# Kernel tuning notes

Measured on AMD Instinct MI355X. Metric: run time of the kernel, lower is better.

Reference implementation:

```python
import jax, jax.numpy as jnp
import numpy as np

N_NODES = 100000


def setup_inputs() -> dict:
    key = jax.random.key(0)
    k1, k2, k3, k4 = jax.random.split(key, 4)
    E = 1600000
    in_dim, out_dim = 256, 64
    h = jax.random.normal(k1, (N_NODES, in_dim), dtype=jnp.float32)
    src = jax.random.randint(k2, (E,), 0, N_NODES, dtype=jnp.int64)
    dst = jax.random.randint(k3, (E,), 0, N_NODES, dtype=jnp.int64)
    W = jax.random.normal(k4, (in_dim, out_dim), dtype=jnp.float32) * (1.0 / np.sqrt(in_dim))
    b = jnp.zeros((out_dim,), dtype=jnp.float32)
    return {"h": h, "src": src, "dst": dst, "W": W, "b": b}


def reference(h, src, dst, W, b):
    # dgl GraphConv, norm='both': out = D_in^{-1/2} A D_out^{-1/2} h W + b
    E = src.shape[0]
    ones = jnp.ones((E,), dtype=h.dtype)
    deg_out = jax.ops.segment_sum(ones, src, num_segments=N_NODES)  # out-degree of src nodes
    deg_in = jax.ops.segment_sum(ones, dst, num_segments=N_NODES)   # in-degree of dst nodes
    norm_src = jnp.clip(deg_out, 1.0, None) ** -0.5                  # [N]
    norm_dst = jnp.clip(deg_in, 1.0, None) ** -0.5                   # [N]
    # in_dim > out_dim: project first (as dgl does), then aggregate small features
    x = (h * norm_src[:, None]) @ W                                  # [N, out_dim]
    msgs = x[src]                                                    # [E, out_dim] gather
    agg = jax.ops.segment_sum(msgs, dst, num_segments=N_NODES)      # [N, out_dim] scatter-add
    out = agg * norm_dst[:, None] + b
    # ReLU; dropout is identity in eval mode
    return jax.nn.relu(out)
```

## Files before the change

### kernel.cpp

```cpp
#include <hip/hip_runtime.h>
#include <hip/hip_fp16.h>

#define N_NODES 100000
#define IN_DIM 256
#define OUT_DIM 64
#define NT 782
#define NSC 512
#define SMAX 3200
#define CAP_F 3072
#define GEMM_BLKS 1563
#define NSPLIT 4
#define A_LD 136
#define FUSED_LDS 47568

typedef _Float16 half8 __attribute__((ext_vector_type(8)));
typedef float f32x4 __attribute__((ext_vector_type(4)));

__global__ __launch_bounds__(256) void init_kernel(int* __restrict__ cursorD,
                                                   int* __restrict__ cursorS) {
    int i = blockIdx.x * 256 + threadIdx.x;
    if (i < NT) { cursorD[i] = 0; cursorS[i] = 0; }
}

__global__ __launch_bounds__(256) void fused_kernel(const int* __restrict__ src,
                                                    const int* __restrict__ dst,
                                                    int* __restrict__ cursorD,
                                                    int* __restrict__ cursorS,
                                                    int* __restrict__ binnedD,
                                                    unsigned char* __restrict__ srcb,
                                                    const float* __restrict__ hmat,
                                                    const float* __restrict__ W,
                                                    __half* __restrict__ xh,
                                                    int E, int chunk) {
    __shared__ char smem[FUSED_LDS];
    const int t = threadIdx.x;
    if (blockIdx.x < NSC) {
        int* sorted            = (int*)(smem);
        int* histD             = (int*)(smem + 12800);
        int* boffD             = (int*)(smem + 15928);
        int* resvD             = (int*)(smem + 19056);
        int* histS             = (int*)(smem + 22184);
        int* boffS             = (int*)(smem + 25312);
        int* resvS             = (int*)(smem + 28440);
        unsigned short* sbin   = (unsigned short*)(smem + 31568);
        unsigned short* sbinS  = (unsigned short*)(smem + 37968);
        unsigned char* sortedB = (unsigned char*)(smem + 44368);
        const int blk = blockIdx.x;
        const int lane = t & 63, wv = t >> 6;
        const int lo = blk * chunk;
        int hiA = lo + chunk; if (hiA > E) hiA = E;
        for (int s0 = lo; s0 < hiA; s0 += SMAX) {
            int m = hiA - s0; if (m > SMAX) m = SMAX;
            for (int i = t; i < NT; i += 256) { histD[i] = 0; histS[i] = 0; }
            __syncthreads();
            for (int k = t; k < m; k += 256) {
                int s = src[s0 + k], d = dst[s0 + k];
                atomicAdd(&histD[d >> 7], 1);
                atomicAdd(&histS[s >> 7], 1);
            }
            __syncthreads();
            if (wv < 2) {
                int* hsrc = (wv == 0) ? histD : histS;
                int* bdst = (wv == 0) ? boffD : boffS;
                int carry = 0;
                for (int r = 0; r < (NT + 63) / 64; ++r) {
                    int i = r * 64 + lane;
                    int v = (i < NT) ? hsrc[i] : 0;
                    int incl = v;
#pragma unroll
                    for (int off = 1; off < 64; off <<= 1) {
                        int y = __shfl_up(incl, off);
                        if (lane >= off) incl += y;
                    }
                    if (i < NT) bdst[i] = carry + incl - v;
                    carry += __shfl(incl, 63);
                }
            }
            __syncthreads();
            for (int i = t; i < NT; i += 256) {
                int hd = histD[i];
                if (hd) resvD[i] = atomicAdd(&cursorD[i], hd);
                int hs = histS[i];
                if (hs) resvS[i] = atomicAdd(&cursorS[i], hs);
                histD[i] = boffD[i];
                histS[i] = boffS[i];
            }
            __syncthreads();
            for (int k = t; k < m; k += 256) {
                int s = src[s0 + k], d = dst[s0 + k];
                int bd = d >> 7;
                int p = atomicAdd(&histD[bd], 1);
                sorted[p] = (s << 7) | (d & 127);
                sbin[p] = (unsigned short)bd;
                int bs = s >> 7;
                int ps = atomicAdd(&histS[bs], 1);
                sortedB[ps] = (unsigned char)(s & 127);
                sbinS[ps] = (unsigned short)bs;
            }
            __syncthreads();
            for (int k = t; k < m; k += 256) {
                int b = sbin[k];
                int loc = resvD[b] + (k - boffD[b]);
                if (loc < CAP_F) binnedD[b * CAP_F + loc] = sorted[k];
                int bs = sbinS[k];
                int locS = resvS[bs] + (k - boffS[bs]);
                if (locS < CAP_F) srcb[bs * CAP_F + locS] = sortedB[k];
            }
            __syncthreads();
        }
    } else {
        _Float16* sA = (_Float16*)(smem);
        _Float16* sB = (_Float16*)(smem + 64 * A_LD * 2);
        const int lane = t & 63;
        const int w = t >> 6;
        const int row0 = (blockIdx.x - NSC) * 64;
        const int m0 = (w & 1) * 32;
        const int n0 = (w >> 1) * 32;

        f32x4 acc00 = {0.f, 0.f, 0.f, 0.f}, acc01 = {0.f, 0.f, 0.f, 0.f};
        f32x4 acc10 = {0.f, 0.f, 0.f, 0.f}, acc11 = {0.f, 0.f, 0.f, 0.f};

        for (int khalf = 0; khalf < 2; ++khalf) {
            const int k0 = khalf * 128;
            __syncthreads();
#pragma unroll
            for (int it = 0; it < 8; ++it) {
                int f = t + it * 256;
                int row = f >> 5;
                int c4 = f & 31;
                int grow = row0 + row; if (grow >= N_NODES) grow = N_NODES - 1;
                float4 v = *(const float4*)(hmat + (size_t)grow * IN_DIM + k0 + c4 * 4);
                _Float16 p[4];
                p[0] = (_Float16)v.x; p[1] = (_Float16)v.y;
                p[2] = (_Float16)v.z; p[3] = (_Float16)v.w;
                *(uint2*)&sA[row * A_LD + c4 * 4] = *(uint2*)p;
            }
            {
                int n = t & 63;
                int kk0 = (t >> 6) * 32;
#pragma unroll
                for (int kb = 0; kb < 8; ++kb) {
                    _Float16 p[4];
#pragma unroll
                    for (int u = 0; u < 4; ++u)
                        p[u] = (_Float16)W[(size_t)(k0 + kk0 + kb * 4 + u) * OUT_DIM + n];
                    *(uint2*)&sB[n * A_LD + kk0 + kb * 4] = *(uint2*)p;
                }
            }
            __syncthreads();
#pragma unroll
            for (int kb = 0; kb < 4; ++kb) {
                int koff = kb * 32 + (lane >> 4) * 8;
                half8 a0 = *(const half8*)&sA[(m0 + (lane & 15)) * A_LD + koff];
                half8 a1 = *(const half8*)&sA[(m0 + 16 + (lane & 15)) * A_LD + koff];
                half8 b0 = *(const half8*)&sB[(n0 + (lane & 15)) * A_LD + koff];
                half8 b1 = *(const half8*)&sB[(n0 + 16 + (lane & 15)) * A_LD + koff];
                acc00 = __builtin_amdgcn_mfma_f32_16x16x32_f16(a0, b0, acc00, 0, 0, 0);
                acc01 = __builtin_amdgcn_mfma_f32_16x16x32_f16(a0, b1, acc01, 0, 0, 0);
                acc10 = __builtin_amdgcn_mfma_f32_16x16x32_f16(a1, b0, acc10, 0, 0, 0);
                acc11 = __builtin_amdgcn_mfma_f32_16x16x32_f16(a1, b1, acc11, 0, 0, 0);
            }
        }

        const int col16 = lane & 15;
        const int rq = (lane >> 4) * 4;
#pragma unroll
        for (int mi = 0; mi < 2; ++mi) {
#pragma unroll
            for (int ni = 0; ni < 2; ++ni) {
                const f32x4 a = (mi == 0) ? (ni == 0 ? acc00 : acc01)
                                          : (ni == 0 ? acc10 : acc11);
                int col = n0 + ni * 16 + col16;
#pragma unroll
                for (int r = 0; r < 4; ++r) {
                    int row = row0 + m0 + mi * 16 + rq + r;
                    if (row < N_NODES)
                        xh[(size_t)row * OUT_DIM + col] = __float2half(a[r]);
                }
            }
        }
    }
}

__global__ __launch_bounds__(256) void scale_kernel(const int* __restrict__ cursorS,
                                                    const unsigned char* __restrict__ srcb,
                                                    __half* __restrict__ xh) {
    __shared__ int h[128];
    __shared__ float sc[128];
    const int bin = blockIdx.x, t = threadIdx.x;
    if (t < 128) h[t] = 0;
    __syncthreads();
    int ms = cursorS[bin]; if (ms > CAP_F) ms = CAP_F;
    const int sbase = bin * CAP_F;
    for (int k = t; k < ms; k += 256) atomicAdd(&h[srcb[sbase + k]], 1);
    __syncthreads();
    if (t < 128) {
        int d = h[t];
        sc[t] = rsqrtf((float)(d < 1 ? 1 : d));
    }
    __syncthreads();
    const int node0 = bin * 128;
    for (int i = t; i < 128 * 16; i += 256) {
        int r = i >> 4, q = i & 15;
        int node = node0 + r;
        if (node < N_NODES) {
            __half2* p = (__half2*)(xh + (size_t)node * OUT_DIM + q * 4);
            float s = sc[r];
            __half2 a0 = p[0], a1 = p[1];
            float2 f0 = __half22float2(a0), f1 = __half22float2(a1);
            __half2 r0, r1;
            r0.x = __float2half(f0.x * s); r0.y = __float2half(f0.y * s);
            r1.x = __float2half(f1.x * s); r1.y = __float2half(f1.y * s);
            p[0] = r0; p[1] = r1;
        }
    }
}

__global__ __launch_bounds__(256) void agg_kernel(const int* __restrict__ cursorD,
                                                  const int* __restrict__ binnedD,
                                                  const __half* __restrict__ xh,
                                                  const float* __restrict__ b,
                                                  float* __restrict__ out) {
    __shared__ int lcsr[CAP_F];
    __shared__ int h[128], cur[128], loff[128], lcnt[128];
    __shared__ int w0tot;
    const int bin = blockIdx.x / NSPLIT;
    const int part = blockIdx.x % NSPLIT;
    const int t = threadIdx.x, lane = t & 63, wv = t >> 6;

    if (t < 128) h[t] = 0;
    __syncthreads();
    const int base = bin * CAP_F;
    int m = cursorD[bin]; if (m > CAP_F) m = CAP_F;
    for (int k = t; k < m; k += 256) atomicAdd(&h[binnedD[base + k] & 127], 1);
    __syncthreads();
    int v = (t < 128) ? h[t] : 0;
    int incl = v;
#pragma unroll
    for (int off = 1; off < 64; off <<= 1) {
        int y = __shfl_up(incl, off);
        if (lane >= off) incl += y;
    }
    if (t == 63) w0tot = incl;
    __syncthreads();
    int excl = incl - v + ((t >= 64 && t < 128) ? w0tot : 0);
    if (t < 128) { loff[t] = excl; lcnt[t] = v; cur[t] = excl; }
    __syncthreads();
    for (int k = t; k < m; k += 256) {
        int rec = binnedD[base + k];
        int p = atomicAdd(&cur[rec & 127], 1);
        lcsr[p] = rec >> 7;
    }
    __syncthreads();

    const int g = lane >> 3;
    const int c = lane & 7;
    for (int idx = 0; idx < 8; ++idx) {
        const int nloc = part * 32 + wv * 8 + idx;
        const int node = bin * 128 + nloc;
        if (node >= N_NODES) continue;
        const int start = loff[nloc];
        const int n = lcnt[nloc];

        float acc[8] = {0.f, 0.f, 0.f, 0.f, 0.f, 0.f, 0.f, 0.f};
        for (int e0 = 0; e0 < n; e0 += 16) {
            int ea = e0 + g;
            int eb = ea + 8;
            bool va = ea < n;
            bool vb = eb < n;
            int sa0 = va ? lcsr[start + ea] : 0;
            float wa = va ? 1.f : 0.f;
            uint4 ra = *(const uint4*)(xh + (size_t)sa0 * OUT_DIM + 8 * c);
            const bool grpb = (e0 + 8) < n;
            uint4 rb;
            float wb = 0.f;
            if (grpb) {
                int sb0 = vb ? lcsr[start + eb] : 0;
                wb = vb ? 1.f : 0.f;
                rb = *(const uint4*)(xh + (size_t)sb0 * OUT_DIM + 8 * c);
            }
            {
                const __half2* hp = (const __half2*)&ra;
#pragma unroll
                for (int p = 0; p < 4; ++p) {
                    float2 f = __half22float2(hp[p]);
                    acc[2 * p]     = fmaf(wa, f.x, acc[2 * p]);
                    acc[2 * p + 1] = fmaf(wa, f.y, acc[2 * p + 1]);
                }
            }
            if (grpb) {
                const __half2* hp = (const __half2*)&rb;
#pragma unroll
                for (int p = 0; p < 4; ++p) {
                    float2 f = __half22float2(hp[p]);
                    acc[2 * p]     = fmaf(wb, f.x, acc[2 * p]);
                    acc[2 * p + 1] = fmaf(wb, f.y, acc[2 * p + 1]);
                }
            }
        }

#pragma unroll
        for (int off = 8; off < 64; off <<= 1) {
#pragma unroll
            for (int p = 0; p < 8; ++p)
                acc[p] += __shfl_xor(acc[p], off);
        }

        if (g == 0) {
            float nrm = rsqrtf((float)(n < 1 ? 1 : n));
            float4 bv0 = *(const float4*)&b[c * 8];
            float4 bv1 = *(const float4*)&b[c * 8 + 4];
            float4 r0, r1;
            r0.x = fmaxf(fmaf(acc[0], nrm, bv0.x), 0.f);
            r0.y = fmaxf(fmaf(acc[1], nrm, bv0.y), 0.f);
            r0.z = fmaxf(fmaf(acc[2], nrm, bv0.z), 0.f);
            r0.w = fmaxf(fmaf(acc[3], nrm, bv0.w), 0.f);
            r1.x = fmaxf(fmaf(acc[4], nrm, bv1.x), 0.f);
            r1.y = fmaxf(fmaf(acc[5], nrm, bv1.y), 0.f);
            r1.z = fmaxf(fmaf(acc[6], nrm, bv1.z), 0.f);
            r1.w = fmaxf(fmaf(acc[7], nrm, bv1.w), 0.f);
            float4* orow = (float4*)(out + (size_t)node * OUT_DIM + c * 8);
            orow[0] = r0;
            orow[1] = r1;
        }
    }
}

extern "C" void kernel_launch(void* const* d_in, const int* in_sizes, int n_in,
                              void* d_out, int out_size, void* d_ws, size_t ws_size,
                              hipStream_t stream) {
    const float* h   = (const float*)d_in[0];
    const int*   src = (const int*)d_in[1];
    const int*   dst = (const int*)d_in[2];
    const float* W   = (const float*)d_in[3];
    const float* b   = (const float*)d_in[4];
    float* out = (float*)d_out;
    const int E = in_sizes[1];
    const int chunkS = (E + NSC - 1) / NSC;

    char* ws = (char*)d_ws;
    int*           cursorD = (int*)(ws);
    int*           cursorS = (int*)(ws + 3328);
    int*           binnedD = (int*)(ws + 6656);
    unsigned char* srcb    = (unsigned char*)(ws + 9615872);
    __half*        xh      = (__half*)(ws + 12018176);

    init_kernel<<<4, 256, 0, stream>>>(cursorD, cursorS);
    fused_kernel<<<NSC + GEMM_BLKS, 256, 0, stream>>>(src, dst, cursorD, cursorS,
                                                      binnedD, srcb, h, W, xh, E, chunkS);
    scale_kernel<<<NT, 256, 0, stream>>>(cursorS, srcb, xh);
    agg_kernel<<<NT * NSPLIT, 256, 0, stream>>>(cursorD, binnedD, xh, b, out);
}
```

Before: 252.5 us.

## Build per-node CSR once in scale kernel, use one wave per node in aggregation

```diff
diff --git a/kernel.cpp b/kernel.cpp
--- a/kernel.cpp
+++ b/kernel.cpp
@@ -9,7 +9,6 @@
 #define SMAX 3200
 #define CAP_F 3072
 #define GEMM_BLKS 1563
-#define NSPLIT 4
 #define A_LD 136
 #define FUSED_LDS 47568
 
@@ -182,12 +181,51 @@
     }
 }
 
-__global__ __launch_bounds__(256) void scale_kernel(const int* __restrict__ cursorS,
-                                                    const unsigned char* __restrict__ srcb,
-                                                    __half* __restrict__ xh) {
-    __shared__ int h[128];
+__global__ __launch_bounds__(256) void tile_scale_kernel(const int* __restrict__ cursorD,
+                                                         const int* __restrict__ cursorS,
+                                                         const int* __restrict__ binnedD,
+                                                         const unsigned char* __restrict__ srcb,
+                                                         int* __restrict__ csr,
+                                                         int* __restrict__ offs,
+                                                         int* __restrict__ cnt,
+                                                         __half* __restrict__ xh) {
+    __shared__ int h[128], cur[128];
+    __shared__ int lcsr[CAP_F];
     __shared__ float sc[128];
-    const int bin = blockIdx.x, t = threadIdx.x;
+    __shared__ int w0tot;
+    const int bin = blockIdx.x, t = threadIdx.x, lane = t & 63;
+    if (t < 128) h[t] = 0;
+    __syncthreads();
+
+    const int base = bin * CAP_F;
+    int m = cursorD[bin]; if (m > CAP_F) m = CAP_F;
+    for (int k = t; k < m; k += 256) atomicAdd(&h[binnedD[base + k] & 127], 1);
+    __syncthreads();
+    int v = (t < 128) ? h[t] : 0;
+    int incl = v;
+#pragma unroll
+    for (int off = 1; off < 64; off <<= 1) {
+        int y = __shfl_up(incl, off);
+        if (lane >= off) incl += y;
+    }
+    if (t == 63) w0tot = incl;
+    __syncthreads();
+    int excl = incl - v + ((t >= 64 && t < 128) ? w0tot : 0);
+    if (t < 128) {
+        cur[t] = excl;
+        int node = bin * 128 + t;
+        if (node < N_NODES) { offs[node] = base + excl; cnt[node] = v; }
+    }
+    __syncthreads();
+    for (int k = t; k < m; k += 256) {
+        int rec = binnedD[base + k];
+        int p = atomicAdd(&cur[rec & 127], 1);
+        lcsr[p] = rec >> 7;
+    }
+    __syncthreads();
+    for (int k = t; k < m; k += 256) csr[base + k] = lcsr[k];
+
+    __syncthreads();
     if (t < 128) h[t] = 0;
     __syncthreads();
     int ms = cursorS[bin]; if (ms > CAP_F) ms = CAP_F;
@@ -216,113 +254,82 @@
     }
 }
 
-__global__ __launch_bounds__(256) void agg_kernel(const int* __restrict__ cursorD,
-                                                  const int* __restrict__ binnedD,
+__global__ __launch_bounds__(256) void agg_kernel(const int* __restrict__ offs,
+                                                  const int* __restrict__ cnt,
+                                                  const int* __restrict__ csr,
                                                   const __half* __restrict__ xh,
                                                   const float* __restrict__ b,
                                                   float* __restrict__ out) {
-    __shared__ int lcsr[CAP_F];
-    __shared__ int h[128], cur[128], loff[128], lcnt[128];
-    __shared__ int w0tot;
-    const int bin = blockIdx.x / NSPLIT;
-    const int part = blockIdx.x % NSPLIT;
-    const int t = threadIdx.x, lane = t & 63, wv = t >> 6;
-
-    if (t < 128) h[t] = 0;
-    __syncthreads();
-    const int base = bin * CAP_F;
-    int m = cursorD[bin]; if (m > CAP_F) m = CAP_F;
-    for (int k = t; k < m; k += 256) atomicAdd(&h[binnedD[base + k] & 127], 1);
-    __syncthreads();
-    int v = (t < 128) ? h[t] : 0;
-    int incl = v;
-#pragma unroll
-    for (int off = 1; off < 64; off <<= 1) {
-        int y = __shfl_up(incl, off);
-        if (lane >= off) incl += y;
-    }
-    if (t == 63) w0tot = incl;
-    __syncthreads();
-    int excl = incl - v + ((t >= 64 && t < 128) ? w0tot : 0);
-    if (t < 128) { loff[t] = excl; lcnt[t] = v; cur[t] = excl; }
-    __syncthreads();
-    for (int k = t; k < m; k += 256) {
-        int rec = binnedD[base + k];
-        int p = atomicAdd(&cur[rec & 127], 1);
-        lcsr[p] = rec >> 7;
-    }
-    __syncthreads();
-
+    const int t = threadIdx.x;
+    const int lane = t & 63;
+    const int wid = t >> 6;
+    const int node = blockIdx.x * 4 + wid;
     const int g = lane >> 3;
     const int c = lane & 7;
-    for (int idx = 0; idx < 8; ++idx) {
-        const int nloc = part * 32 + wv * 8 + idx;
-        const int node = bin * 128 + nloc;
-        if (node >= N_NODES) continue;
-        const int start = loff[nloc];
-        const int n = lcnt[nloc];
-
-        float acc[8] = {0.f, 0.f, 0.f, 0.f, 0.f, 0.f, 0.f, 0.f};
-        for (int e0 = 0; e0 < n; e0 += 16) {
-            int ea = e0 + g;
-            int eb = ea + 8;
-            bool va = ea < n;
-            bool vb = eb < n;
-            int sa0 = va ? lcsr[start + ea] : 0;
-            float wa = va ? 1.f : 0.f;
-            uint4 ra = *(const uint4*)(xh + (size_t)sa0 * OUT_DIM + 8 * c);
-            const bool grpb = (e0 + 8) < n;
-            uint4 rb;
-            float wb = 0.f;
-            if (grpb) {
-                int sb0 = vb ? lcsr[start + eb] : 0;
-                wb = vb ? 1.f : 0.f;
-                rb = *(const uint4*)(xh + (size_t)sb0 * OUT_DIM + 8 * c);
-            }
-            {
-                const __half2* hp = (const __half2*)&ra;
-#pragma unroll
-                for (int p = 0; p < 4; ++p) {
-                    float2 f = __half22float2(hp[p]);
-                    acc[2 * p]     = fmaf(wa, f.x, acc[2 * p]);
-                    acc[2 * p + 1] = fmaf(wa, f.y, acc[2 * p + 1]);
-                }
-            }
-            if (grpb) {
-                const __half2* hp = (const __half2*)&rb;
-#pragma unroll
-                for (int p = 0; p < 4; ++p) {
-                    float2 f = __half22float2(hp[p]);
-                    acc[2 * p]     = fmaf(wb, f.x, acc[2 * p]);
-                    acc[2 * p + 1] = fmaf(wb, f.y, acc[2 * p + 1]);
-                }
-            }
-        }
-
-#pragma unroll
-        for (int off = 8; off < 64; off <<= 1) {
-#pragma unroll
-            for (int p = 0; p < 8; ++p)
-                acc[p] += __shfl_xor(acc[p], off);
-        }
-
-        if (g == 0) {
-            float nrm = rsqrtf((float)(n < 1 ? 1 : n));
-            float4 bv0 = *(const float4*)&b[c * 8];
-            float4 bv1 = *(const float4*)&b[c * 8 + 4];
-            float4 r0, r1;
-            r0.x = fmaxf(fmaf(acc[0], nrm, bv0.x), 0.f);
-            r0.y = fmaxf(fmaf(acc[1], nrm, bv0.y), 0.f);
-            r0.z = fmaxf(fmaf(acc[2], nrm, bv0.z), 0.f);
-            r0.w = fmaxf(fmaf(acc[3], nrm, bv0.w), 0.f);
-            r1.x = fmaxf(fmaf(acc[4], nrm, bv1.x), 0.f);
-            r1.y = fmaxf(fmaf(acc[5], nrm, bv1.y), 0.f);
-            r1.z = fmaxf(fmaf(acc[6], nrm, bv1.z), 0.f);
-            r1.w = fmaxf(fmaf(acc[7], nrm, bv1.w), 0.f);
-            float4* orow = (float4*)(out + (size_t)node * OUT_DIM + c * 8);
-            orow[0] = r0;
-            orow[1] = r1;
-        }
+
+    const int start = offs[node];
+    const int n = cnt[node];
+
+    float acc[8] = {0.f, 0.f, 0.f, 0.f, 0.f, 0.f, 0.f, 0.f};
+    for (int e0 = 0; e0 < n; e0 += 16) {
+        int ea = e0 + g;
+        int eb = ea + 8;
+        bool va = ea < n;
+        bool vb = eb < n;
+        int sa0 = va ? csr[start + ea] : 0;
+        float wa = va ? 1.f : 0.f;
+        uint4 ra = *(const uint4*)(xh + (size_t)sa0 * OUT_DIM + 8 * c);
+        const bool grpb = (e0 + 8) < n;
+        uint4 rb;
+        float wb = 0.f;
+        if (grpb) {
+            int sb0 = vb ? csr[start + eb] : 0;
+            wb = vb ? 1.f : 0.f;
+            rb = *(const uint4*)(xh + (size_t)sb0 * OUT_DIM + 8 * c);
+        }
+        {
+            const __half2* hp = (const __half2*)&ra;
+#pragma unroll
+            for (int p = 0; p < 4; ++p) {
+                float2 f = __half22float2(hp[p]);
+                acc[2 * p]     = fmaf(wa, f.x, acc[2 * p]);
+                acc[2 * p + 1] = fmaf(wa, f.y, acc[2 * p + 1]);
+            }
+        }
+        if (grpb) {
+            const __half2* hp = (const __half2*)&rb;
+#pragma unroll
+            for (int p = 0; p < 4; ++p) {
+                float2 f = __half22float2(hp[p]);
+                acc[2 * p]     = fmaf(wb, f.x, acc[2 * p]);
+                acc[2 * p + 1] = fmaf(wb, f.y, acc[2 * p + 1]);
+            }
+        }
+    }
+
+#pragma unroll
+    for (int off = 8; off < 64; off <<= 1) {
+#pragma unroll
+        for (int p = 0; p < 8; ++p)
+            acc[p] += __shfl_xor(acc[p], off);
+    }
+
+    if (g == 0) {
+        float nrm = rsqrtf((float)(n < 1 ? 1 : n));
+        float4 bv0 = *(const float4*)&b[c * 8];
+        float4 bv1 = *(const float4*)&b[c * 8 + 4];
+        float4 r0, r1;
+        r0.x = fmaxf(fmaf(acc[0], nrm, bv0.x), 0.f);
+        r0.y = fmaxf(fmaf(acc[1], nrm, bv0.y), 0.f);
+        r0.z = fmaxf(fmaf(acc[2], nrm, bv0.z), 0.f);
+        r0.w = fmaxf(fmaf(acc[3], nrm, bv0.w), 0.f);
+        r1.x = fmaxf(fmaf(acc[4], nrm, bv1.x), 0.f);
+        r1.y = fmaxf(fmaf(acc[5], nrm, bv1.y), 0.f);
+        r1.z = fmaxf(fmaf(acc[6], nrm, bv1.z), 0.f);
+        r1.w = fmaxf(fmaf(acc[7], nrm, bv1.w), 0.f);
+        float4* orow = (float4*)(out + (size_t)node * OUT_DIM + c * 8);
+        orow[0] = r0;
+        orow[1] = r1;
     }
 }
 
@@ -342,12 +349,16 @@
     int*           cursorD = (int*)(ws);
     int*           cursorS = (int*)(ws + 3328);
     int*           binnedD = (int*)(ws + 6656);
+    int*           csr     = binnedD;
     unsigned char* srcb    = (unsigned char*)(ws + 9615872);
-    __half*        xh      = (__half*)(ws + 12018176);
+    int*           offs    = (int*)(ws + 12018176);
+    int*           cntA    = (int*)(ws + 12418176);
+    __half*        xh      = (__half*)(ws + 12818176);
 
     init_kernel<<<4, 256, 0, stream>>>(cursorD, cursorS);
     fused_kernel<<<NSC + GEMM_BLKS, 256, 0, stream>>>(src, dst, cursorD, cursorS,
                                                       binnedD, srcb, h, W, xh, E, chunkS);
-    scale_kernel<<<NT, 256, 0, stream>>>(cursorS, srcb, xh);
-    agg_kernel<<<NT * NSPLIT, 256, 0, stream>>>(cursorD, binnedD, xh, b, out);
-}
+    tile_scale_kernel<<<NT, 256, 0, stream>>>(cursorD, cursorS, binnedD, srcb,
+                                              csr, offs, cntA, xh);
+    agg_kernel<<<N_NODES / 4, 256, 0, stream>>>(offs, cntA, csr, xh, b, out);
+}
```

Result: slower. 262.4 us (+3.9%).
